# Kernel optimization log

Measured on AMD Instinct MI355X. Metric: run time of the kernel, lower is better.

## Reference

```python
import jax, jax.numpy as jnp
import numpy as np

B, D, H, O, E, TOP_K = 1024, 1024, 2048, 1024, 8, 2


def setup_inputs() -> dict:
    key = jax.random.key(0)
    ks = jax.random.split(key, 8)
    s = 0.02
    return {
        "x":  jax.random.normal(ks[0], (B, D), dtype=jnp.float32),
        "Wr": jax.random.normal(ks[1], (D, E), dtype=jnp.float32) * s,
        "br": jnp.zeros((E,), dtype=jnp.float32),
        "W1": jax.random.normal(ks[2], (E, D, H), dtype=jnp.float32) * s,
        "b1": jnp.zeros((E, H), dtype=jnp.float32),
        "W2": jax.random.normal(ks[3], (E, H, H), dtype=jnp.float32) * s,
        "b2": jnp.zeros((E, H), dtype=jnp.float32),
        "W3": jax.random.normal(ks[4], (E, H, O), dtype=jnp.float32) * s,
        "b3": jnp.zeros((E, O), dtype=jnp.float32),
    }


def reference(x, Wr, br, W1, b1, W2, b2, W3, b3):
    # --- router: softmax -> top-k -> renormalize selected weights ---
    logits = x @ Wr + br                      # [B, E]
    probs = jax.nn.softmax(logits, axis=-1)
    w, ids = jax.lax.top_k(probs, TOP_K)      # [B, K], [B, K]
    w = w / (jnp.sum(w, axis=-1, keepdims=True) + 1e-6)

    # --- expert MLPs (depth=2: in->h, relu, h->h, relu, h->out) ---
    h = jax.nn.relu(jnp.einsum('bd,edh->beh', x, W1) + b1)   # [B, E, H]
    h = jax.nn.relu(jnp.einsum('beh,ehg->beg', h, W2) + b2)  # [B, E, H]
    y_e = jnp.einsum('beg,ego->beo', h, W3) + b3             # [B, E, O]

    # --- weighted scatter-combine: comb[b,e] = sum_k w[b,k] * [ids[b,k]==e] ---
    comb = jnp.sum(jax.nn.one_hot(ids, E, dtype=x.dtype) * w[..., None], axis=1)  # [B, E]
    out = jnp.einsum('beo,be->bo', y_e, comb)                # [B, O]
    return out
```

## Files before the change

### kernel.cpp

```cpp
#include <hip/hip_runtime.h>
#include <hip/hip_bf16.h>

#define BT 1024
#define DD 1024
#define HH 2048
#define OO 1024
#define EE 8
#define RMAX 3072

typedef __bf16 bf16x8 __attribute__((ext_vector_type(8)));
typedef float  f32x4  __attribute__((ext_vector_type(4)));

__device__ __forceinline__ void cp16(void* l, const void* g) {
    __builtin_amdgcn_global_load_lds(
        (const __attribute__((address_space(1))) void*)g,
        (__attribute__((address_space(3))) void*)l, 16, 0, 0);
}


__global__ __launch_bounds__(256) void router_kernel(
    const float* __restrict__ x, const float* __restrict__ Wr, const float* __restrict__ br,
    int* __restrict__ counts, int* __restrict__ elist,
    int* __restrict__ tok_e, int* __restrict__ tok_p, float* __restrict__ tok_w)
{
    int b = blockIdx.x;
    int tid = threadIdx.x;
    float acc[EE];
#pragma unroll
    for (int e = 0; e < EE; ++e) acc[e] = 0.f;
    const float* xr = x + (size_t)b * DD;
    for (int d = tid; d < DD; d += 256) {
        float xv = xr[d];
#pragma unroll
        for (int e = 0; e < EE; ++e) acc[e] += xv * Wr[d * EE + e];
    }
    __shared__ float red[4][EE];
    int lane = tid & 63, wv = tid >> 6;
#pragma unroll
    for (int e = 0; e < EE; ++e) {
        float v = acc[e];
#pragma unroll
        for (int o = 32; o > 0; o >>= 1) v += __shfl_down(v, o, 64);
        if (lane == 0) red[wv][e] = v;
    }
    __syncthreads();
    if (tid == 0) {
        float lg[EE];
#pragma unroll
        for (int e = 0; e < EE; ++e) lg[e] = red[0][e] + red[1][e] + red[2][e] + red[3][e] + br[e];
        float mx = lg[0];
#pragma unroll
        for (int e = 1; e < EE; ++e) mx = fmaxf(mx, lg[e]);
        float s = 0.f, p[EE];
#pragma unroll
        for (int e = 0; e < EE; ++e) { p[e] = expf(lg[e] - mx); s += p[e]; }
        float inv = 1.f / s;
#pragma unroll
        for (int e = 0; e < EE; ++e) p[e] *= inv;
        int i0 = 0; float b0 = p[0];
#pragma unroll
        for (int e = 1; e < EE; ++e) if (p[e] > b0) { b0 = p[e]; i0 = e; }
        int i1 = -1; float b1v = -1.f;
#pragma unroll
        for (int e = 0; e < EE; ++e) if (e != i0 && p[e] > b1v) { b1v = p[e]; i1 = e; }
        float s2 = b0 + b1v + 1e-6f;
        float w0 = b0 / s2, w1 = b1v / s2;
        int p0 = atomicAdd(&counts[i0], 1);
        int p1 = atomicAdd(&counts[i1], 1);
        elist[i0 * 1024 + p0] = b;
        elist[i1 * 1024 + p1] = b;
        tok_e[2 * b] = i0; tok_e[2 * b + 1] = i1;
        tok_p[2 * b] = p0; tok_p[2 * b + 1] = p1;
        tok_w[2 * b] = w0; tok_w[2 * b + 1] = w1;
    }
}

__global__ void offsets_kernel(const int* __restrict__ counts, int* __restrict__ off)
{
    if (threadIdx.x == 0 && blockIdx.x == 0) {
        int a = 0;
        for (int e = 0; e < EE; ++e) {
            off[e] = a;
            a += ((counts[e] + 127) >> 7) << 7;
        }
        off[EE] = a;
    }
}

__global__ __launch_bounds__(256) void gather_kernel(
    const float* __restrict__ x, const int* __restrict__ counts, const int* __restrict__ off,
    const int* __restrict__ elist, __bf16* __restrict__ Xg)
{
    int e = blockIdx.y;
    int chunk = blockIdx.x >> 2;
    int rg = blockIdx.x & 3;
    int cnt = counts[e];
    if (chunk * 128 >= cnt) return;
    int base = off[e] + chunk * 128 + rg * 32;
    int tid = threadIdx.x;
    for (int it = 0; it < 32; ++it) {
        int slot = chunk * 128 + rg * 32 + it;
        __bf16 v[4];
        if (slot < cnt) {
            int tok = elist[e * 1024 + slot];
            const float4 f = *(const float4*)(x + (size_t)tok * DD + tid * 4);
            v[0] = (__bf16)f.x; v[1] = (__bf16)f.y; v[2] = (__bf16)f.z; v[3] = (__bf16)f.w;
        } else {
            v[0] = v[1] = v[2] = v[3] = (__bf16)0.f;
        }
        *(uint2*)(Xg + (size_t)(base + it) * DD + tid * 4) = *(uint2*)v;
    }
}

template <int K, int N, int KSPLIT>
__global__ __launch_bounds__(256) void gemm_splitk(
    const __bf16* __restrict__ A, const float* __restrict__ Wall,
    float* __restrict__ P, const int* __restrict__ counts, const int* __restrict__ off)
{
    constexpr int TN = 64;
    constexpr int KC = K / KSPLIT;
    int e = blockIdx.z;
    int mt = blockIdx.y / KSPLIT;
    int kp = blockIdx.y % KSPLIT;
    int nt = blockIdx.x;
    int cnt = counts[e];
    if (mt * 128 >= cnt) return;
    int row0 = off[e] + mt * 128;

    const __bf16* Ab = A + (size_t)row0 * K + (size_t)kp * KC;
    const float*  Wp = Wall + (size_t)e * K * N + (size_t)kp * KC * N + nt * TN;
    float* Pp = P + (size_t)kp * RMAX * N;

    __shared__ __bf16 As[128 * 32];
    __shared__ __bf16 Bs[64 * 40];

    int tid = threadIdx.x;
    int wave = tid >> 6, lane = tid & 63;
    int m = lane & 15, q = lane >> 4;
    int wm = (wave >> 1) * 64, wn = (wave & 1) * 32;

    int ar = (tid >> 6) * 16 + ((tid & 63) >> 2);
    int k8 = (tid & 3) * 8;
    int bn = tid & 63;
    int bkc = (tid >> 6) * 8;

    f32x4 acc[4][2] = {};

    for (int k0 = 0; k0 < KC; k0 += 32) {
        cp16(&As[ar * 32 + k8],        Ab + (size_t)ar * K + k0 + k8);
        cp16(&As[(64 + ar) * 32 + k8], Ab + (size_t)(64 + ar) * K + k0 + k8);
        {
            __bf16 t8[8];
            const float* p = Wp + (size_t)(k0 + bkc) * N + bn;
#pragma unroll
            for (int g = 0; g < 8; ++g) t8[g] = (__bf16)p[(size_t)g * N];
            *(uint4*)(&Bs[bn * 40 + bkc]) = *(uint4*)t8;
        }
        __syncthreads();

        bf16x8 af[4], bfr[2];
#pragma unroll
        for (int i = 0; i < 4; ++i)
            af[i] = *(bf16x8*)(&As[(wm + i * 16 + m) * 32 + q * 8]);
#pragma unroll
        for (int j = 0; j < 2; ++j)
            bfr[j] = *(bf16x8*)(&Bs[(wn + j * 16 + m) * 40 + q * 8]);
#pragma unroll
        for (int i = 0; i < 4; ++i)
#pragma unroll
            for (int j = 0; j < 2; ++j)
                acc[i][j] = __builtin_amdgcn_mfma_f32_16x16x32_bf16(af[i], bfr[j], acc[i][j], 0, 0, 0);
        __syncthreads();
    }

    int colbase = nt * TN + wn;
#pragma unroll
    for (int j = 0; j < 2; ++j) {
        int col = colbase + j * 16 + m;
#pragma unroll
        for (int i = 0; i < 4; ++i) {
            int rbase = row0 + wm + i * 16 + q * 4;
#pragma unroll
            for (int r = 0; r < 4; ++r)
                Pp[(size_t)(rbase + r) * N + col] = acc[i][j][r];
        }
    }
}

template <int N, int KSPLIT>
__global__ __launch_bounds__(256) void reduce_relu(
    const float* __restrict__ P, const float* __restrict__ bias,
    __bf16* __restrict__ H, const int* __restrict__ off)
{
    int row = blockIdx.y;
    if (row >= off[EE]) return;
    int e = 0;
#pragma unroll
    for (int t = 0; t < EE - 1; ++t) if (row >= off[t + 1]) e = t + 1;
    int col = blockIdx.x * 1024 + threadIdx.x * 4;
    f32x4 s = *(const f32x4*)(P + (size_t)row * N + col);
#pragma unroll
    for (int k = 1; k < KSPLIT; ++k)
        s += *(const f32x4*)(P + (size_t)k * RMAX * N + (size_t)row * N + col);
    s += *(const f32x4*)(bias + (size_t)e * N + col);
    __bf16 o[4];
#pragma unroll
    for (int c = 0; c < 4; ++c) o[c] = (__bf16)fmaxf(s[c], 0.f);
    *(uint2*)(H + (size_t)row * N + col) = *(uint2*)o;
}

__global__ __launch_bounds__(256) void combine_kernel(
    const float* __restrict__ P3, const float* __restrict__ b3, const int* __restrict__ off,
    const int* __restrict__ tok_e, const int* __restrict__ tok_p,
    const float* __restrict__ tok_w, float* __restrict__ out)
{
    int b = blockIdx.x, t = threadIdx.x;
    int e0 = tok_e[2 * b], e1 = tok_e[2 * b + 1];
    int r0 = off[e0] + tok_p[2 * b];
    int r1 = off[e1] + tok_p[2 * b + 1];
    float w0 = tok_w[2 * b], w1 = tok_w[2 * b + 1];
    int col = t * 4;
    f32x4 s0 = *(const f32x4*)(P3 + (size_t)r0 * OO + col);
    f32x4 s1 = *(const f32x4*)(P3 + (size_t)r1 * OO + col);
#pragma unroll
    for (int k = 1; k < 4; ++k) {
        s0 += *(const f32x4*)(P3 + (size_t)k * RMAX * OO + (size_t)r0 * OO + col);
        s1 += *(const f32x4*)(P3 + (size_t)k * RMAX * OO + (size_t)r1 * OO + col);
    }
    s0 += *(const f32x4*)(b3 + (size_t)e0 * OO + col);
    s1 += *(const f32x4*)(b3 + (size_t)e1 * OO + col);
    f32x4 o = s0 * w0 + s1 * w1;
    *(f32x4*)(out + (size_t)b * OO + col) = o;
}

extern "C" void kernel_launch(void* const* d_in, const int* in_sizes, int n_in,
                              void* d_out, int out_size, void* d_ws, size_t ws_size,
                              hipStream_t stream)
{
    (void)in_sizes; (void)n_in; (void)out_size; (void)ws_size;
    const float* x  = (const float*)d_in[0];
    const float* Wr = (const float*)d_in[1];
    const float* br = (const float*)d_in[2];
    const float* W1 = (const float*)d_in[3];
    const float* b1 = (const float*)d_in[4];
    const float* W2 = (const float*)d_in[5];
    const float* b2 = (const float*)d_in[6];
    const float* W3 = (const float*)d_in[7];
    const float* b3 = (const float*)d_in[8];
    float* out = (float*)d_out;

    char* ws = (char*)d_ws;
    int*    counts = (int*)(ws + 0);
    int*    off    = (int*)(ws + 256);
    int*    tok_e  = (int*)(ws + 1024);
    int*    tok_p  = (int*)(ws + 9216);
    float*  tok_w  = (float*)(ws + 17408);
    int*    elist  = (int*)(ws + 25600);
    __bf16* Xg     = (__bf16*)(ws + 65536);
    __bf16* H1     = (__bf16*)(ws + 6356992);
    __bf16* H2     = (__bf16*)(ws + 18939904);
    float*  P1     = (float*)(ws + 31522816);
    float*  P2     = (float*)(ws + 81854464);
    float*  P3     = (float*)(ws + 132186112);

    hipMemsetAsync(counts, 0, 256, stream);
    router_kernel<<<1024, 256, 0, stream>>>(x, Wr, br, counts, elist, tok_e, tok_p, tok_w);
    offsets_kernel<<<1, 64, 0, stream>>>(counts, off);
    gather_kernel<<<dim3(32, 8), 256, 0, stream>>>(x, counts, off, elist, Xg);

    gemm_splitk<1024, 2048, 2><<<dim3(32, 16, 8), 256, 0, stream>>>(Xg, W1, P1, counts, off);
    reduce_relu<2048, 2><<<dim3(2, RMAX), 256, 0, stream>>>(P1, b1, H1, off);
    gemm_splitk<2048, 2048, 2><<<dim3(32, 16, 8), 256, 0, stream>>>(H1, W2, P2, counts, off);
    reduce_relu<2048, 2><<<dim3(2, RMAX), 256, 0, stream>>>(P2, b2, H2, off);
    gemm_splitk<2048, 1024, 4><<<dim3(16, 32, 8), 256, 0, stream>>>(H2, W3, P3, counts, off);

    combine_kernel<<<1024, 256, 0, stream>>>(P3, b3, off, tok_e, tok_p, tok_w, out);
}
```

Before: 469.2 us.

## Drop split-K, fuse bias/ReLU epilogue, double-buffer GEMM tiles

Removes split-K partial sums and the separate reduce_relu kernels, so each GEMM writes biased, activated bf16 (or fp32 for the last layer) output directly. The combine kernel now reads one output buffer with no bias add. Adds double-buffered LDS with register-staged weight loads to overlap the next tile's fetch with the current MFMAs. It also reorders the grid so expert varies fastest and uses a 32-wide N tile for the last layer. This cuts fp32 partial-sum traffic and kernel launches, at the cost of fewer blocks per GEMM and longer serial K loops.

```diff
diff --git a/kernel.cpp b/kernel.cpp
--- a/kernel.cpp
+++ b/kernel.cpp
@@ -112,105 +112,115 @@
     }
 }
 
-template <int K, int N, int KSPLIT>
-__global__ __launch_bounds__(256) void gemm_splitk(
+template <int K, int N, int TN, bool RELU, bool OUT_BF16>
+__global__ __launch_bounds__(256) void gemm_fused(
     const __bf16* __restrict__ A, const float* __restrict__ Wall,
-    float* __restrict__ P, const int* __restrict__ counts, const int* __restrict__ off)
-{
-    constexpr int TN = 64;
-    constexpr int KC = K / KSPLIT;
-    int e = blockIdx.z;
-    int mt = blockIdx.y / KSPLIT;
-    int kp = blockIdx.y % KSPLIT;
-    int nt = blockIdx.x;
+    const float* __restrict__ bias, void* __restrict__ OutV,
+    const int* __restrict__ counts, const int* __restrict__ off)
+{
+    constexpr int NSTEPS = K / 32;
+    constexpr int NJ  = TN / 32;
+    constexpr int BLD = TN / 8;
+
+    int e  = blockIdx.x & 7;
+    int nt = blockIdx.x >> 3;
+    int mt = blockIdx.y;
     int cnt = counts[e];
     if (mt * 128 >= cnt) return;
     int row0 = off[e] + mt * 128;
 
-    const __bf16* Ab = A + (size_t)row0 * K + (size_t)kp * KC;
-    const float*  Wp = Wall + (size_t)e * K * N + (size_t)kp * KC * N + nt * TN;
-    float* Pp = P + (size_t)kp * RMAX * N;
-
-    __shared__ __bf16 As[128 * 32];
-    __shared__ __bf16 Bs[64 * 40];
+    const __bf16* Ab = A + (size_t)row0 * K;
+    const float*  Wp = Wall + (size_t)e * K * N + nt * TN;
+
+    __shared__ __bf16 As[2][128 * 32];
+    __shared__ __bf16 Bs[2][TN * 40];
 
     int tid = threadIdx.x;
     int wave = tid >> 6, lane = tid & 63;
     int m = lane & 15, q = lane >> 4;
-    int wm = (wave >> 1) * 64, wn = (wave & 1) * 32;
-
-    int ar = (tid >> 6) * 16 + ((tid & 63) >> 2);
-    int k8 = (tid & 3) * 8;
-    int bn = tid & 63;
-    int bkc = (tid >> 6) * 8;
-
-    f32x4 acc[4][2] = {};
-
-    for (int k0 = 0; k0 < KC; k0 += 32) {
-        cp16(&As[ar * 32 + k8],        Ab + (size_t)ar * K + k0 + k8);
-        cp16(&As[(64 + ar) * 32 + k8], Ab + (size_t)(64 + ar) * K + k0 + k8);
-        {
-            __bf16 t8[8];
-            const float* p = Wp + (size_t)(k0 + bkc) * N + bn;
-#pragma unroll
-            for (int g = 0; g < 8; ++g) t8[g] = (__bf16)p[(size_t)g * N];
-            *(uint4*)(&Bs[bn * 40 + bkc]) = *(uint4*)t8;
-        }
-        __syncthreads();
-
-        bf16x8 af[4], bfr[2];
+    int wm = (wave >> 1) * 64, wn = (wave & 1) * (TN / 2);
+
+    int ar = wave * 16 + (lane >> 2);
+    int k8 = (lane & 3) * 8;
+    int bn  = (TN == 64) ? (tid & 63) : (tid & 31);
+    int bkc = (TN == 64) ? ((tid >> 6) * 8) : ((tid >> 5) * 4);
+
+    float breg[BLD];
+    f32x4 acc[4][NJ] = {};
+
+    auto issueA = [&](int t, int buf) {
+        const __bf16* src = Ab + t * 32;
+        cp16(&As[buf][ar * 32 + k8],        src + (size_t)ar * K + k8);
+        cp16(&As[buf][(64 + ar) * 32 + k8], src + (size_t)(64 + ar) * K + k8);
+    };
+    auto loadB = [&](int t) {
+        const float* p = Wp + (size_t)(t * 32 + bkc) * N + bn;
+#pragma unroll
+        for (int g = 0; g < BLD; ++g) breg[g] = p[(size_t)g * N];
+    };
+    auto writeB = [&](int buf) {
+        __bf16 t8[BLD];
+#pragma unroll
+        for (int g = 0; g < BLD; ++g) t8[g] = (__bf16)breg[g];
+        if constexpr (TN == 64) *(uint4*)(&Bs[buf][bn * 40 + bkc]) = *(uint4*)t8;
+        else                    *(uint2*)(&Bs[buf][bn * 40 + bkc]) = *(uint2*)t8;
+    };
+
+    issueA(0, 0);
+    loadB(0);
+    __syncthreads();
+    writeB(0);
+    __syncthreads();
+
+    for (int t = 0; t < NSTEPS; ++t) {
+        int cur = t & 1;
+        if (t + 1 < NSTEPS) {
+            issueA(t + 1, cur ^ 1);
+            loadB(t + 1);
+        }
+        bf16x8 af[4], bfr[NJ];
 #pragma unroll
         for (int i = 0; i < 4; ++i)
-            af[i] = *(bf16x8*)(&As[(wm + i * 16 + m) * 32 + q * 8]);
-#pragma unroll
-        for (int j = 0; j < 2; ++j)
-            bfr[j] = *(bf16x8*)(&Bs[(wn + j * 16 + m) * 40 + q * 8]);
+            af[i] = *(bf16x8*)(&As[cur][(wm + i * 16 + m) * 32 + q * 8]);
+#pragma unroll
+        for (int j = 0; j < NJ; ++j)
+            bfr[j] = *(bf16x8*)(&Bs[cur][(wn + j * 16 + m) * 40 + q * 8]);
 #pragma unroll
         for (int i = 0; i < 4; ++i)
 #pragma unroll
-            for (int j = 0; j < 2; ++j)
+            for (int j = 0; j < NJ; ++j)
                 acc[i][j] = __builtin_amdgcn_mfma_f32_16x16x32_bf16(af[i], bfr[j], acc[i][j], 0, 0, 0);
-        __syncthreads();
-    }
-
+        if (t + 1 < NSTEPS) {
+            __syncthreads();
+            writeB(cur ^ 1);
+            __syncthreads();
+        }
+    }
+
+    const float* bp = bias + (size_t)e * N;
     int colbase = nt * TN + wn;
 #pragma unroll
-    for (int j = 0; j < 2; ++j) {
+    for (int j = 0; j < NJ; ++j) {
         int col = colbase + j * 16 + m;
+        float bv = bp[col];
 #pragma unroll
         for (int i = 0; i < 4; ++i) {
             int rbase = row0 + wm + i * 16 + q * 4;
 #pragma unroll
-            for (int r = 0; r < 4; ++r)
-                Pp[(size_t)(rbase + r) * N + col] = acc[i][j][r];
-        }
-    }
-}
-
-template <int N, int KSPLIT>
-__global__ __launch_bounds__(256) void reduce_relu(
-    const float* __restrict__ P, const float* __restrict__ bias,
-    __bf16* __restrict__ H, const int* __restrict__ off)
-{
-    int row = blockIdx.y;
-    if (row >= off[EE]) return;
-    int e = 0;
-#pragma unroll
-    for (int t = 0; t < EE - 1; ++t) if (row >= off[t + 1]) e = t + 1;
-    int col = blockIdx.x * 1024 + threadIdx.x * 4;
-    f32x4 s = *(const f32x4*)(P + (size_t)row * N + col);
-#pragma unroll
-    for (int k = 1; k < KSPLIT; ++k)
-        s += *(const f32x4*)(P + (size_t)k * RMAX * N + (size_t)row * N + col);
-    s += *(const f32x4*)(bias + (size_t)e * N + col);
-    __bf16 o[4];
-#pragma unroll
-    for (int c = 0; c < 4; ++c) o[c] = (__bf16)fmaxf(s[c], 0.f);
-    *(uint2*)(H + (size_t)row * N + col) = *(uint2*)o;
+            for (int r = 0; r < 4; ++r) {
+                float v = acc[i][j][r] + bv;
+                if constexpr (RELU) v = fmaxf(v, 0.f);
+                if constexpr (OUT_BF16)
+                    ((__bf16*)OutV)[(size_t)(rbase + r) * N + col] = (__bf16)v;
+                else
+                    ((float*)OutV)[(size_t)(rbase + r) * N + col] = v;
+            }
+        }
+    }
 }
 
 __global__ __launch_bounds__(256) void combine_kernel(
-    const float* __restrict__ P3, const float* __restrict__ b3, const int* __restrict__ off,
+    const float* __restrict__ Y, const int* __restrict__ off,
     const int* __restrict__ tok_e, const int* __restrict__ tok_p,
     const float* __restrict__ tok_w, float* __restrict__ out)
 {
@@ -220,15 +230,8 @@
     int r1 = off[e1] + tok_p[2 * b + 1];
     float w0 = tok_w[2 * b], w1 = tok_w[2 * b + 1];
     int col = t * 4;
-    f32x4 s0 = *(const f32x4*)(P3 + (size_t)r0 * OO + col);
-    f32x4 s1 = *(const f32x4*)(P3 + (size_t)r1 * OO + col);
-#pragma unroll
-    for (int k = 1; k < 4; ++k) {
-        s0 += *(const f32x4*)(P3 + (size_t)k * RMAX * OO + (size_t)r0 * OO + col);
-        s1 += *(const f32x4*)(P3 + (size_t)k * RMAX * OO + (size_t)r1 * OO + col);
-    }
-    s0 += *(const f32x4*)(b3 + (size_t)e0 * OO + col);
-    s1 += *(const f32x4*)(b3 + (size_t)e1 * OO + col);
+    f32x4 s0 = *(const f32x4*)(Y + (size_t)r0 * OO + col);
+    f32x4 s1 = *(const f32x4*)(Y + (size_t)r1 * OO + col);
     f32x4 o = s0 * w0 + s1 * w1;
     *(f32x4*)(out + (size_t)b * OO + col) = o;
 }
@@ -259,20 +262,16 @@
     __bf16* Xg     = (__bf16*)(ws + 65536);
     __bf16* H1     = (__bf16*)(ws + 6356992);
     __bf16* H2     = (__bf16*)(ws + 18939904);
-    float*  P1     = (float*)(ws + 31522816);
-    float*  P2     = (float*)(ws + 81854464);
-    float*  P3     = (float*)(ws + 132186112);
+    float*  Y      = (float*)(ws + 31522816);
 
     hipMemsetAsync(counts, 0, 256, stream);
     router_kernel<<<1024, 256, 0, stream>>>(x, Wr, br, counts, elist, tok_e, tok_p, tok_w);
     offsets_kernel<<<1, 64, 0, stream>>>(counts, off);
     gather_kernel<<<dim3(32, 8), 256, 0, stream>>>(x, counts, off, elist, Xg);
 
-    gemm_splitk<1024, 2048, 2><<<dim3(32, 16, 8), 256, 0, stream>>>(Xg, W1, P1, counts, off);
-    reduce_relu<2048, 2><<<dim3(2, RMAX), 256, 0, stream>>>(P1, b1, H1, off);
-    gemm_splitk<2048, 2048, 2><<<dim3(32, 16, 8), 256, 0, stream>>>(H1, W2, P2, counts, off);
-    reduce_relu<2048, 2><<<dim3(2, RMAX), 256, 0, stream>>>(P2, b2, H2, off);
-    gemm_splitk<2048, 1024, 4><<<dim3(16, 32, 8), 256, 0, stream>>>(H2, W3, P3, counts, off);
-
-    combine_kernel<<<1024, 256, 0, stream>>>(P3, b3, off, tok_e, tok_p, tok_w, out);
-}
+    gemm_fused<1024, 2048, 64, true,  true ><<<dim3(256, 8), 256, 0, stream>>>(Xg, W1, b1, (void*)H1, counts, off);
+    gemm_fused<2048, 2048, 64, true,  true ><<<dim3(256, 8), 256, 0, stream>>>(H1, W2, b2, (void*)H2, counts, off);
+    gemm_fused<2048, 1024, 32, false, false><<<dim3(256, 8), 256, 0, stream>>>(H2, W3, b3, (void*)Y,  counts, off);
+
+    combine_kernel<<<1024, 256, 0, stream>>>(Y, off, tok_e, tok_p, tok_w, out);
+}
```

New measurement: 439.5 us. -6.3%, faster.
